# Kernel optimization log

Hardware: AMD Instinct MI355X
Metric: run time of the kernel (lower is better)

The kernel has to match this reference:

```python
import jax, jax.numpy as jnp
import numpy as np

B, N = 4096, 128
STATE_DIM, GOAL_DIM, OBSTACLE_DIM = 6, 6, 4
VEH = 2 * STATE_DIM + GOAL_DIM  # 18


def setup_inputs() -> dict:
    key = jax.random.key(0)
    ks = jax.random.split(key, 8)
    s = lambda k, shp, fan: jax.random.normal(k, shp, jnp.float32) / np.sqrt(fan)
    return {
        "obs": jax.random.normal(ks[0], (B, 138), jnp.float32),
        "obstacles": jax.random.uniform(ks[1], (B, 5, N), jnp.float32),
        "act": jax.random.normal(ks[2], (B, 2), jnp.float32),
        "ow1": s(ks[3], (22, 256), 22),
        "ob1": jnp.zeros((256,), jnp.float32),
        "ow2": s(ks[4], (256, 256), 256),
        "ob2": jnp.zeros((256,), jnp.float32),
        "qw1": s(ks[5], (396, 256), 396),
        "qb1": jnp.zeros((256,), jnp.float32),
        "qw2": s(ks[6], (256, 256), 256),
        "qb2": jnp.zeros((256,), jnp.float32),
        "qw3": s(ks[7], (256, 1), 256),
        "qb3": jnp.zeros((1,), jnp.float32),
    }


def reference(obs, obstacles, act, ow1, ob1, ow2, ob2, qw1, qb1, qw2, qb2, qw3, qb3):
    # obs: [B, 138]; obstacles: [B, obstacle_dim+1, N]; act: [B, 2]
    veh = obs[:, :VEH]                                 # [B, 18]
    obst_data = obstacles[:, :OBSTACLE_DIM, :]         # [B, 4, N]
    mask = obstacles[:, -1, :]                         # [B, N]
    # per-obstacle features: concat broadcast vehicle state with obstacle data -> [B, N, 22]
    x = jnp.concatenate(
        [jnp.broadcast_to(veh[:, None, :], (veh.shape[0], obst_data.shape[2], VEH)),
         obst_data.transpose(0, 2, 1)], axis=-1)
    # shared obstacle MLP (ReLU on both layers, incl. output_activation)
    h = jax.nn.relu(jnp.einsum("bnf,fh->bnh", x, ow1) + ob1)
    h = jax.nn.relu(jnp.einsum("bnh,hk->bnk", h, ow2) + ob2)  # [B, N, 256]
    # masked sum-pool over obstacle axis
    pooled = jnp.einsum("bnh,bn->bh", h, mask)         # [B, 256]
    comb = jnp.concatenate([obs, pooled, act], axis=-1)  # [B, 396]
    q = jax.nn.relu(comb @ qw1 + qb1)
    q = jax.nn.relu(q @ qw2 + qb2)
    q = q @ qw3 + qb3                                   # [B, 1]
    return jnp.squeeze(q, -1)
```

## Files before the change

### kernel.cpp

```cpp
#include <hip/hip_runtime.h>
#include <hip/hip_bf16.h>


typedef __attribute__((ext_vector_type(8))) short short8;
typedef __attribute__((ext_vector_type(4))) float f32x4;

#define MFMA16(A, B, C) __builtin_amdgcn_mfma_f32_16x16x32_bf16(A, B, C, 0, 0, 0)

__device__ __forceinline__ unsigned short f2b(float f) {
  __hip_bfloat16 h = __float2bfloat16(f);
  return __builtin_bit_cast(unsigned short, h);
}
__device__ __forceinline__ float b2f(unsigned short u) {
  unsigned v = ((unsigned)u) << 16;
  return __builtin_bit_cast(float, v);
}
__device__ __forceinline__ unsigned pk2f(float a, float b) {
  unsigned ua = __builtin_bit_cast(unsigned, a) + 0x8000u;
  unsigned ub = __builtin_bit_cast(unsigned, b) + 0x8000u;
  return __builtin_amdgcn_perm(ub, ua, 0x07060302u);
}

__global__ __launch_bounds__(256) void pack_weights(
    const float* __restrict__ ow1, const float* __restrict__ ow2,
    const float* __restrict__ qw1, const float* __restrict__ qw2,
    unsigned short* __restrict__ ow1q, unsigned short* __restrict__ ow2p,
    unsigned short* __restrict__ qw1h, unsigned short* __restrict__ qw1l,
    unsigned short* __restrict__ qw2h, unsigned short* __restrict__ qw2l) {
  int i = blockIdx.x * 256 + threadIdx.x;
  if (i < 8192) {
    int j = i & 7;
    int l15 = (i >> 3) & 15;
    int quad = (i >> 7) & 3;
    int mt = (i >> 9) & 15;
    int k = quad * 8 + j;
    float v = (k < 22) ? ow1[k * 256 + (mt * 16 + l15)] : 0.f;
    ow1q[i] = f2b(v);
  }
  if (i < 65536) {
    int j = i & 7;
    int n = (i >> 3) & 255;
    int qq = i >> 11;
    int k = (qq >> 2) * 32 + (qq & 3) * 8 + j;
    ow2p[i] = f2b(ow2[k * 256 + n]);
    float w = qw2[k * 256 + n];
    unsigned short h = f2b(w);
    qw2h[i] = h;
    qw2l[i] = f2b(w - b2f(h));
  }
  if (i < 106496) {
    int j = i & 7;
    int n = (i >> 3) & 255;
    int qq = i >> 11;
    int k = (qq >> 2) * 32 + (qq & 3) * 8 + j;
    float w = (k < 396) ? qw1[k * 256 + n] : 0.f;
    unsigned short h = f2b(w);
    qw1h[i] = h;
    qw1l[i] = f2b(w - b2f(h));
  }
}

#define XSTR 40
#define HSTR 264

__global__ __launch_bounds__(512, 4) void obstacle_kernel(
    const float* __restrict__ obs, const float* __restrict__ obstacles,
    const unsigned short* __restrict__ ow1q,
    const unsigned short* __restrict__ ow2p,
    const float* __restrict__ ob1, const float* __restrict__ ob2,
    unsigned short* __restrict__ poolH, unsigned short* __restrict__ poolL) {
  __shared__ unsigned short xs[128 * XSTR];
  __shared__ unsigned short h1[128 * HSTR];
  __shared__ float maskS[128];
  __shared__ unsigned short vehB[32];

  const int b = blockIdx.x;
  const int tid = threadIdx.x;

  if (tid < 18) vehB[tid] = f2b(obs[b * 138 + tid]);
  if (tid < 128) maskS[tid] = obstacles[b * 640 + 512 + tid];
  __syncthreads();

  if (tid < 256) {
    int n = tid >> 1;
    int half = tid & 1;
    unsigned short* wr = &xs[n * XSTR + half * 16];
    if (half == 0) {
      unsigned short r01[16];
#pragma unroll
      for (int k = 0; k < 16; k++) r01[k] = vehB[k];
      *(short8*)(wr + 0) = *(short8*)&r01[0];
      *(short8*)(wr + 8) = *(short8*)&r01[8];
    } else {
      unsigned short r2[8];
      r2[0] = vehB[16];
      r2[1] = vehB[17];
#pragma unroll
      for (int d = 0; d < 4; d++)
        r2[2 + d] = f2b(obstacles[b * 640 + d * 128 + n]);
      r2[6] = 0; r2[7] = 0;
      *(short8*)(wr + 0) = *(short8*)&r2[0];
      short8 z = {0, 0, 0, 0, 0, 0, 0, 0};
      *(short8*)(wr + 8) = z;
    }
  }
  __syncthreads();

  const int wave = tid >> 6;
  const int lane = tid & 63;
  const int quad = lane >> 4;
  const int l15 = lane & 15;

  {
    const unsigned short* wp = &ow1q[wave * 1024 + quad * 128 + l15 * 8];
    short8 wfr[2];
#pragma unroll
    for (int i = 0; i < 2; i++) wfr[i] = *(const short8*)(wp + i * 512);

    const unsigned short* bxp = &xs[l15 * XSTR + quad * 8];
    short8 bx[8];
#pragma unroll
    for (int nt = 0; nt < 8; nt++)
      bx[nt] = *(const short8*)(bxp + nt * 16 * XSTR);

    unsigned short* wrb = &h1[l15 * HSTR + wave * 32 + quad * 4];

#pragma unroll
    for (int i = 0; i < 2; i++) {
      f32x4 cinit = *(const f32x4*)&ob1[wave * 32 + i * 16 + quad * 4];
      f32x4 acc1[8];
#pragma unroll
      for (int nt = 0; nt < 8; nt++) acc1[nt] = MFMA16(wfr[i], bx[nt], cinit);
#pragma unroll
      for (int nt = 0; nt < 8; nt++) {
        float v0 = fmaxf(acc1[nt][0], 0.f);
        float v1 = fmaxf(acc1[nt][1], 0.f);
        float v2 = fmaxf(acc1[nt][2], 0.f);
        float v3 = fmaxf(acc1[nt][3], 0.f);
        uint2 pk;
        pk.x = pk2f(v0, v1);
        pk.y = pk2f(v2, v3);
        *(uint2*)(wrb + nt * 16 * HSTR + i * 16) = pk;
      }
    }
  }
  __syncthreads();

  f32x4 acc[8][2];
#pragma unroll
  for (int t = 0; t < 2; t++) {
    float bv = ob2[wave * 32 + t * 16 + l15];
    f32x4 bvec = {bv, bv, bv, bv};
#pragma unroll
    for (int mt = 0; mt < 8; mt++) acc[mt][t] = bvec;
  }

  const unsigned short* bp = &ow2p[(quad * 256 + wave * 32 + l15) * 8];
  const unsigned short* h1r = &h1[l15 * HSTR + quad * 8];
  short8 bcur[2], bnxt[2];
#pragma unroll
  for (int t = 0; t < 2; t++) bcur[t] = *(const short8*)(bp + t * 128);

#pragma unroll 1
  for (int kb = 0; kb < 8; kb++) {
    if (kb < 7) {
#pragma unroll
      for (int t = 0; t < 2; t++)
        bnxt[t] = *(const short8*)(bp + 8192 + t * 128);
    }
    short8 afr[8];
#pragma unroll
    for (int mt = 0; mt < 8; mt++)
      afr[mt] = *(const short8*)(h1r + mt * 16 * HSTR);
#pragma unroll
    for (int mt = 0; mt < 8; mt++)
#pragma unroll
      for (int t = 0; t < 2; t++) acc[mt][t] = MFMA16(afr[mt], bcur[t], acc[mt][t]);
    bp += 8192;
    h1r += 32;
    if (kb < 7) {
#pragma unroll
      for (int t = 0; t < 2; t++) bcur[t] = bnxt[t];
    }
  }

  f32x4 mk[8];
  const float* mkp = &maskS[quad * 4];
#pragma unroll
  for (int mt = 0; mt < 8; mt++) mk[mt] = *(const f32x4*)(mkp + mt * 16);

#pragma unroll
  for (int t = 0; t < 2; t++) {
    float s = 0.f;
#pragma unroll
    for (int mt = 0; mt < 8; mt++) {
#pragma unroll
      for (int r = 0; r < 4; r++) {
        float v = fmaxf(acc[mt][t][r], 0.f);
        s = fmaf(mk[mt][r], v, s);
      }
    }
    s += __shfl_xor(s, 16);
    s += __shfl_xor(s, 32);
    if (quad == 0) {
      int n = wave * 32 + t * 16 + l15;
      unsigned short sh = (unsigned short)(__builtin_bit_cast(unsigned, s) >> 16);
      poolH[b * 256 + n] = sh;
      poolL[b * 256 + n] = f2b(s - b2f(sh));
    }
  }
}

__global__ __launch_bounds__(1024) void head_mfma(
    const float* __restrict__ obs, const float* __restrict__ act,
    const unsigned short* __restrict__ poolH,
    const unsigned short* __restrict__ poolL,
    const unsigned short* __restrict__ qw1h,
    const unsigned short* __restrict__ qw1l,
    const unsigned short* __restrict__ qw2h,
    const unsigned short* __restrict__ qw2l,
    const float* __restrict__ qb1, const float* __restrict__ qb2,
    const float* __restrict__ qw3, const float* __restrict__ qb3,
    float* __restrict__ out) {
  const int CSTR = 424;
  const int HSTRQ = 264;
  __shared__ unsigned short combH[16 * 424], combL[16 * 424];
  __shared__ unsigned short h1H[16 * 264], h1L[16 * 264];
  __shared__ float wred[16][16];

  const int tid = threadIdx.x;
  const int r0 = blockIdx.x * 16;

  for (int idx = tid; idx < 16 * 416; idx += 1024) {
    int m = idx / 416;
    int k = idx - m * 416;
    unsigned short hi, lo;
    if (k < 138) {
      float v = obs[(r0 + m) * 138 + k];
      hi = f2b(v);
      lo = f2b(v - b2f(hi));
    } else if (k < 394) {
      hi = poolH[(r0 + m) * 256 + (k - 138)];
      lo = poolL[(r0 + m) * 256 + (k - 138)];
    } else if (k < 396) {
      float v = act[(r0 + m) * 2 + (k - 394)];
      hi = f2b(v);
      lo = f2b(v - b2f(hi));
    } else {
      hi = 0; lo = 0;
    }
    combH[m * CSTR + k] = hi;
    combL[m * CSTR + k] = lo;
  }
  __syncthreads();

  const int wave = tid >> 6;
  const int lane = tid & 63;
  const int quad = lane >> 4;
  const int l15 = lane & 15;
  const int n = wave * 16 + l15;

  f32x4 acc = {0.f, 0.f, 0.f, 0.f}, accm = {0.f, 0.f, 0.f, 0.f};
#pragma unroll 1
  for (int kb = 0; kb < 13; kb++) {
    int ao = l15 * CSTR + kb * 32 + quad * 8;
    short8 ah = *(const short8*)&combH[ao];
    short8 al = *(const short8*)&combL[ao];
    int off = ((kb * 4 + quad) * 256 + n) * 8;
    short8 bh = *(const short8*)&qw1h[off];
    short8 bl = *(const short8*)&qw1l[off];
    acc = MFMA16(ah, bh, acc);
    accm = MFMA16(ah, bl, accm);
    accm = MFMA16(al, bh, accm);
  }
  {
    float bias = qb1[n];
#pragma unroll
    for (int r = 0; r < 4; r++) {
      int m = quad * 4 + r;
      float v = fmaxf(acc[r] + accm[r] + bias, 0.f);
      unsigned short hi = f2b(v);
      h1H[m * HSTRQ + n] = hi;
      h1L[m * HSTRQ + n] = f2b(v - b2f(hi));
    }
  }
  __syncthreads();

  f32x4 a2 = {0.f, 0.f, 0.f, 0.f}, a2m = {0.f, 0.f, 0.f, 0.f};
#pragma unroll 1
  for (int kb = 0; kb < 8; kb++) {
    int ao = l15 * HSTRQ + kb * 32 + quad * 8;
    short8 ah = *(const short8*)&h1H[ao];
    short8 al = *(const short8*)&h1L[ao];
    int off = ((kb * 4 + quad) * 256 + n) * 8;
    short8 bh = *(const short8*)&qw2h[off];
    short8 bl = *(const short8*)&qw2l[off];
    a2 = MFMA16(ah, bh, a2);
    a2m = MFMA16(ah, bl, a2m);
    a2m = MFMA16(al, bh, a2m);
  }

  {
    float w3 = qw3[n];
    float qb2n = qb2[n];
#pragma unroll
    for (int r = 0; r < 4; r++) {
      float v = fmaxf(a2[r] + a2m[r] + qb2n, 0.f);
      float s = v * w3;
      s += __shfl_xor(s, 1);
      s += __shfl_xor(s, 2);
      s += __shfl_xor(s, 4);
      s += __shfl_xor(s, 8);
      if (l15 == 0) wred[wave][quad * 4 + r] = s;
    }
  }
  __syncthreads();
  if (tid < 16) {
    float s = qb3[0];
#pragma unroll
    for (int w = 0; w < 16; w++) s += wred[w][tid];
    out[r0 + tid] = s;
  }
}

extern "C" void kernel_launch(void* const* d_in, const int* in_sizes, int n_in,
                              void* d_out, int out_size, void* d_ws, size_t ws_size,
                              hipStream_t stream) {
  const float* obs       = (const float*)d_in[0];
  const float* obstacles = (const float*)d_in[1];
  const float* act       = (const float*)d_in[2];
  const float* ow1       = (const float*)d_in[3];
  const float* ob1       = (const float*)d_in[4];
  const float* ow2       = (const float*)d_in[5];
  const float* ob2       = (const float*)d_in[6];
  const float* qw1       = (const float*)d_in[7];
  const float* qb1       = (const float*)d_in[8];
  const float* qw2       = (const float*)d_in[9];
  const float* qb2       = (const float*)d_in[10];
  const float* qw3       = (const float*)d_in[11];
  const float* qb3       = (const float*)d_in[12];
  float* out = (float*)d_out;

  unsigned short* ow1q = (unsigned short*)d_ws;
  unsigned short* ow2p = ow1q + 8192;
  unsigned short* qw1h = ow2p + 65536;
  unsigned short* qw1l = qw1h + 106496;
  unsigned short* qw2h = qw1l + 106496;
  unsigned short* qw2l = qw2h + 65536;
  unsigned short* poolH = qw2l + 65536;
  unsigned short* poolL = poolH + 1048576;

  pack_weights<<<416, 256, 0, stream>>>(ow1, ow2, qw1, qw2, ow1q, ow2p, qw1h,
                                        qw1l, qw2h, qw2l);
  obstacle_kernel<<<4096, 512, 0, stream>>>(obs, obstacles, ow1q, ow2p, ob1,
                                            ob2, poolH, poolL);
  head_mfma<<<256, 1024, 0, stream>>>(obs, act, poolH, poolL, qw1h, qw1l,
                                      qw2h, qw2l, qb1, qb2, qw3, qb3, out);
}
```

Before: 166.8 us.

## Switch obstacle layer-2 GEMM to 32x32x16 MFMA with 2x2 wave tiling

Layer 2 of the obstacle MLP now uses 32x32x16 bf16 MFMA instead of 16x16x32. Each wave computes a 64x64 tile (two M-halves by four N-groups) rather than all 128 rows by 32 columns, and the ow2 weights are repacked to match. This is meant to cut LDS A-fragment reads per MFMA and improve operand reuse. The cost is a shared-memory partial-sum buffer and an extra barrier to combine the two M-halves of the masked pooling.

```diff
diff --git a/kernel.cpp b/kernel.cpp
--- a/kernel.cpp
+++ b/kernel.cpp
@@ -4,8 +4,10 @@
 
 typedef __attribute__((ext_vector_type(8))) short short8;
 typedef __attribute__((ext_vector_type(4))) float f32x4;
+typedef __attribute__((ext_vector_type(16))) float f32x16;
 
 #define MFMA16(A, B, C) __builtin_amdgcn_mfma_f32_16x16x32_bf16(A, B, C, 0, 0, 0)
+#define MFMA32(A, B, C) __builtin_amdgcn_mfma_f32_32x32x16_bf16(A, B, C, 0, 0, 0)
 
 __device__ __forceinline__ unsigned short f2b(float f) {
   __hip_bfloat16 h = __float2bfloat16(f);
@@ -39,14 +41,23 @@
   }
   if (i < 65536) {
     int j = i & 7;
-    int n = (i >> 3) & 255;
-    int qq = i >> 11;
-    int k = (qq >> 2) * 32 + (qq & 3) * 8 + j;
-    ow2p[i] = f2b(ow2[k * 256 + n]);
-    float w = qw2[k * 256 + n];
-    unsigned short h = f2b(w);
-    qw2h[i] = h;
-    qw2l[i] = f2b(w - b2f(h));
+    {
+      int col = (i >> 3) & 31;
+      int hi = (i >> 8) & 1;
+      int ks = (i >> 9) & 15;
+      int nt = (i >> 13) & 7;
+      int k = ks * 16 + hi * 8 + j;
+      ow2p[i] = f2b(ow2[k * 256 + nt * 32 + col]);
+    }
+    {
+      int n = (i >> 3) & 255;
+      int qq = i >> 11;
+      int k = (qq >> 2) * 32 + (qq & 3) * 8 + j;
+      float w = qw2[k * 256 + n];
+      unsigned short h = f2b(w);
+      qw2h[i] = h;
+      qw2l[i] = f2b(w - b2f(h));
+    }
   }
   if (i < 106496) {
     int j = i & 7;
@@ -69,9 +80,10 @@
     const unsigned short* __restrict__ ow2p,
     const float* __restrict__ ob1, const float* __restrict__ ob2,
     unsigned short* __restrict__ poolH, unsigned short* __restrict__ poolL) {
-  __shared__ unsigned short xs[128 * XSTR];
-  __shared__ unsigned short h1[128 * HSTR];
+  __shared__ __align__(16) unsigned short xs[128 * XSTR];
+  __shared__ __align__(16) unsigned short h1[128 * HSTR];
   __shared__ float maskS[128];
+  __shared__ float poolP[2][256];
   __shared__ unsigned short vehB[32];
 
   const int b = blockIdx.x;
@@ -146,68 +158,71 @@
   }
   __syncthreads();
 
-  f32x4 acc[8][2];
-#pragma unroll
-  for (int t = 0; t < 2; t++) {
-    float bv = ob2[wave * 32 + t * 16 + l15];
-    f32x4 bvec = {bv, bv, bv, bv};
-#pragma unroll
-    for (int mt = 0; mt < 8; mt++) acc[mt][t] = bvec;
-  }
-
-  const unsigned short* bp = &ow2p[(quad * 256 + wave * 32 + l15) * 8];
-  const unsigned short* h1r = &h1[l15 * HSTR + quad * 8];
-  short8 bcur[2], bnxt[2];
-#pragma unroll
-  for (int t = 0; t < 2; t++) bcur[t] = *(const short8*)(bp + t * 128);
-
+  const int mg = wave >> 2;
+  const int ng = wave & 3;
+  const int hi5 = lane >> 5;
+  const int l31 = lane & 31;
+
+  f32x16 acc[2][2];
+#pragma unroll
+  for (int ntl = 0; ntl < 2; ntl++) {
+    float bv = ob2[ng * 64 + ntl * 32 + l31];
+    f32x16 cinit;
+#pragma unroll
+    for (int r = 0; r < 16; r++) cinit[r] = bv;
+    acc[0][ntl] = cinit;
+    acc[1][ntl] = cinit;
+  }
+
+  const unsigned short* bp = &ow2p[ng * 16384 + hi5 * 256 + l31 * 8];
+  const unsigned short* ar = &h1[(mg * 64 + l31) * HSTR + hi5 * 8];
+
+  short8 bc0 = *(const short8*)bp;
+  short8 bc1 = *(const short8*)(bp + 8192);
 #pragma unroll 1
-  for (int kb = 0; kb < 8; kb++) {
-    if (kb < 7) {
-#pragma unroll
-      for (int t = 0; t < 2; t++)
-        bnxt[t] = *(const short8*)(bp + 8192 + t * 128);
-    }
-    short8 afr[8];
-#pragma unroll
-    for (int mt = 0; mt < 8; mt++)
-      afr[mt] = *(const short8*)(h1r + mt * 16 * HSTR);
-#pragma unroll
-    for (int mt = 0; mt < 8; mt++)
-#pragma unroll
-      for (int t = 0; t < 2; t++) acc[mt][t] = MFMA16(afr[mt], bcur[t], acc[mt][t]);
-    bp += 8192;
-    h1r += 32;
-    if (kb < 7) {
-#pragma unroll
-      for (int t = 0; t < 2; t++) bcur[t] = bnxt[t];
-    }
-  }
-
-  f32x4 mk[8];
-  const float* mkp = &maskS[quad * 4];
-#pragma unroll
-  for (int mt = 0; mt < 8; mt++) mk[mt] = *(const f32x4*)(mkp + mt * 16);
-
-#pragma unroll
-  for (int t = 0; t < 2; t++) {
+  for (int ks = 0; ks < 16; ks++) {
+    short8 bn0, bn1;
+    if (ks < 15) {
+      bn0 = *(const short8*)(bp + 512);
+      bn1 = *(const short8*)(bp + 8704);
+    }
+    short8 a0 = *(const short8*)ar;
+    short8 a1 = *(const short8*)(ar + 32 * HSTR);
+    acc[0][0] = MFMA32(a0, bc0, acc[0][0]);
+    acc[1][0] = MFMA32(a1, bc0, acc[1][0]);
+    acc[0][1] = MFMA32(a0, bc1, acc[0][1]);
+    acc[1][1] = MFMA32(a1, bc1, acc[1][1]);
+    bp += 512;
+    ar += 16;
+    if (ks < 15) { bc0 = bn0; bc1 = bn1; }
+  }
+
+  f32x4 mk[2][4];
+#pragma unroll
+  for (int mt = 0; mt < 2; mt++)
+#pragma unroll
+    for (int g = 0; g < 4; g++)
+      mk[mt][g] = *(const f32x4*)&maskS[mg * 64 + mt * 32 + g * 8 + hi5 * 4];
+
+#pragma unroll
+  for (int ntl = 0; ntl < 2; ntl++) {
     float s = 0.f;
 #pragma unroll
-    for (int mt = 0; mt < 8; mt++) {
-#pragma unroll
-      for (int r = 0; r < 4; r++) {
-        float v = fmaxf(acc[mt][t][r], 0.f);
-        s = fmaf(mk[mt][r], v, s);
-      }
-    }
-    s += __shfl_xor(s, 16);
+    for (int mt = 0; mt < 2; mt++)
+#pragma unroll
+      for (int g = 0; g < 4; g++)
+#pragma unroll
+        for (int r = 0; r < 4; r++)
+          s = fmaf(mk[mt][g][r], fmaxf(acc[mt][ntl][g * 4 + r], 0.f), s);
     s += __shfl_xor(s, 32);
-    if (quad == 0) {
-      int n = wave * 32 + t * 16 + l15;
-      unsigned short sh = (unsigned short)(__builtin_bit_cast(unsigned, s) >> 16);
-      poolH[b * 256 + n] = sh;
-      poolL[b * 256 + n] = f2b(s - b2f(sh));
-    }
+    if (lane < 32) poolP[mg][ng * 64 + ntl * 32 + l31] = s;
+  }
+  __syncthreads();
+  if (tid < 256) {
+    float s = poolP[0][tid] + poolP[1][tid];
+    unsigned short sh = (unsigned short)(__builtin_bit_cast(unsigned, s) >> 16);
+    poolH[b * 256 + tid] = sh;
+    poolL[b * 256 + tid] = f2b(s - b2f(sh));
   }
 }
 
```

Result: slower. 182.0 us (+9.1%).
